# Optimization experiments

Measured on AMD Instinct MI355X. Metric: run time of the kernel, lower is better.

The kernel has to match this reference:

```python
import jax, jax.numpy as jnp
import numpy as np

N = 200000
D_NODE = 256
D_EDGE = 128
D_OUT = 256
J = 17


def setup_inputs() -> dict:
    key = jax.random.key(0)
    ks = jax.random.split(key, 16)
    s = 0.02
    return {
        "nodes_1": jax.random.normal(ks[0], (N, D_NODE), jnp.float32),
        "nodes_2": jax.random.normal(ks[1], (N, D_NODE), jnp.float32),
        "edges": jax.random.normal(ks[2], (N, D_EDGE), jnp.float32),
        "node_types_1": jax.random.randint(ks[3], (N,), 0, J),
        "node_types_2": jax.random.randint(ks[4], (N,), 0, J),
        # per-joint linear stacks (torch Linear weight [out,in] stored transposed as [in,out])
        "W1": jax.random.normal(ks[5], (J, D_NODE, D_OUT), jnp.float32) * s,
        "b1": jax.random.normal(ks[6], (J, D_OUT), jnp.float32) * s,
        "W2": jax.random.normal(ks[7], (J, D_NODE, D_OUT), jnp.float32) * s,
        "b2": jax.random.normal(ks[8], (J, D_OUT), jnp.float32) * s,
        "We": jax.random.normal(ks[9], (D_EDGE, D_OUT), jnp.float32) * s,
        "be": jax.random.normal(ks[10], (D_OUT,), jnp.float32) * s,
        "Wout": jax.random.normal(ks[11], (3 * D_OUT, D_OUT), jnp.float32) * s,
        "bout": jax.random.normal(ks[12], (D_OUT,), jnp.float32) * s,
    }


def _per_type_linear(nodes, types, W, b):
    # Equivalent to: for each joint i, tmp[types==i] = nodes[types==i] @ W[i] + b[i]
    out = jnp.zeros((nodes.shape[0], W.shape[2]), nodes.dtype)
    for i in range(W.shape[0]):  # small fixed loop over joint types
        yi = nodes @ W[i] + b[i]
        out = jnp.where((types == i)[:, None], yi, out)
    return out


def reference(nodes_1, nodes_2, edges, node_types_1, node_types_2,
              W1, b1, W2, b2, We, be, Wout, bout):
    tmp_1 = _per_type_linear(nodes_1, node_types_1, W1, b1)
    tmp_2 = _per_type_linear(nodes_2, node_types_2, W2, b2)
    e = edges @ We + be
    cat = jnp.concatenate([tmp_1, tmp_2, e], axis=1)  # [N, 3*D_OUT]
    h = jax.nn.relu(cat) @ Wout + bout
    return jax.nn.relu(h)
```

## Files before the change

kernel.cpp:

```cpp
#include <hip/hip_runtime.h>


#define J_TYPES 17
#define PAIRS   (J_TYPES * J_TYPES)
#define DN      256
#define DE      128
#define DO      256
#define TILE    64
#define LDA     264
#define LDE     136

typedef short bf16x8 __attribute__((ext_vector_type(8)));
typedef float f32x4  __attribute__((ext_vector_type(4)));

#define BAR() asm volatile("s_waitcnt lgkmcnt(0)\n\ts_barrier" ::: "memory")

__device__ __forceinline__ unsigned short f2bf(float x) {
  unsigned u = __float_as_uint(x);
  return (unsigned short)((u + 0x7fffu + ((u >> 16) & 1u)) >> 16);
}

__device__ __forceinline__ unsigned cvtpk(float lo, float hi) {
  unsigned r;
  asm("v_cvt_pk_bf16_f32 %0, %1, %2" : "=v"(r) : "v"(lo), "v"(hi));
  return r;
}

__global__ void prep_w_k(const float* __restrict__ W1, const float* __restrict__ W2,
                         const float* __restrict__ We, const float* __restrict__ Wout,
                         unsigned short* __restrict__ W1t, unsigned short* __restrict__ W2t,
                         unsigned short* __restrict__ Wet, unsigned short* __restrict__ Ut) {
  const int SZW = J_TYPES * 65536;
  const int total = SZW * 2 + DE * DO + 3 * 65536;
  for (int o = blockIdx.x * blockDim.x + threadIdx.x; o < total;
       o += gridDim.x * blockDim.x) {
    int idx = o;
    if (idx < SZW) {
      int j = idx >> 16, r = idx & 65535;
      int i = r & 7, lane = (r >> 3) & 63, t = r >> 9;
      int k32 = t & 7, colt = t >> 3;
      int col = colt * 16 + (lane & 15);
      int k = k32 * 32 + ((lane >> 4) << 3) + i;
      W1t[idx] = f2bf(W1[((size_t)j * 256 + k) * 256 + col]);
    } else if ((idx -= SZW) < SZW) {
      int j = idx >> 16, r = idx & 65535;
      int i = r & 7, lane = (r >> 3) & 63, t = r >> 9;
      int k32 = t & 7, colt = t >> 3;
      int col = colt * 16 + (lane & 15);
      int k = k32 * 32 + ((lane >> 4) << 3) + i;
      W2t[idx] = f2bf(W2[((size_t)j * 256 + k) * 256 + col]);
    } else if ((idx -= SZW) < DE * DO) {
      int r = idx;
      int i = r & 7, lane = (r >> 3) & 63, t = r >> 9;
      int k32 = t & 3, colt = t >> 2;
      int col = colt * 16 + (lane & 15);
      int k = k32 * 32 + ((lane >> 4) << 3) + i;
      Wet[idx] = f2bf(We[(size_t)k * 256 + col]);
    } else {
      idx -= DE * DO;
      int p = idx >> 16, r = idx & 65535;
      int i = r & 7, lane = (r >> 3) & 63, t = r >> 9;
      int k32 = t & 7, colt = t >> 3;
      int col = colt * 16 + (lane & 15);
      int k = k32 * 32 + ((lane >> 4) << 3) + i;
      Ut[idx] = f2bf(Wout[((size_t)p * 256 + k) * 256 + col]);
    }
  }
}

__global__ void hist_k(const int* __restrict__ ty1, const int* __restrict__ ty2,
                       int* __restrict__ cnt, int N) {
  __shared__ int h[PAIRS];
  for (int i = threadIdx.x; i < PAIRS; i += blockDim.x) h[i] = 0;
  __syncthreads();
  for (int i = blockIdx.x * blockDim.x + threadIdx.x; i < N;
       i += gridDim.x * blockDim.x)
    atomicAdd(&h[ty1[i] * J_TYPES + ty2[i]], 1);
  __syncthreads();
  for (int i = threadIdx.x; i < PAIRS; i += blockDim.x) {
    int v = h[i];
    if (v) atomicAdd(&cnt[i], v);
  }
}

__global__ void scan_tiles_k(const int* __restrict__ cnt, int* __restrict__ seg,
                             int* __restrict__ tpair, int* __restrict__ tstart,
                             int* __restrict__ tnr, int* __restrict__ ntl) {
  __shared__ int s1[512], s2[512];
  int t = threadIdx.x;
  int c  = (t < PAIRS) ? cnt[t] : 0;
  int nt = (c + TILE - 1) / TILE;
  s1[t] = c; s2[t] = nt;
  __syncthreads();
  for (int o = 1; o < 512; o <<= 1) {
    int v1 = (t >= o) ? s1[t - o] : 0;
    int v2 = (t >= o) ? s2[t - o] : 0;
    __syncthreads();
    s1[t] += v1; s2[t] += v2;
    __syncthreads();
  }
  if (t < PAIRS) {
    int segstart = s1[t] - c;
    int tbase    = s2[t] - nt;
    seg[t] = segstart;
    for (int i = 0; i < nt; ++i) {
      tpair[tbase + i]  = t;
      tstart[tbase + i] = segstart + i * TILE;
      int rem = c - i * TILE;
      tnr[tbase + i] = rem < TILE ? rem : TILE;
    }
  }
  if (t == 511) ntl[0] = s2[511];
}

__global__ void scatter_k(const int* __restrict__ ty1, const int* __restrict__ ty2,
                          const int* __restrict__ seg, int* __restrict__ c2,
                          int* __restrict__ ridx, int N) {
  __shared__ int lh[PAIRS], lb[PAIRS];
  int chunk = (N + gridDim.x - 1) / gridDim.x;
  int lo = blockIdx.x * chunk;
  int hi = lo + chunk; if (hi > N) hi = N;
  for (int i = threadIdx.x; i < PAIRS; i += blockDim.x) lh[i] = 0;
  __syncthreads();
  for (int i = lo + threadIdx.x; i < hi; i += blockDim.x)
    atomicAdd(&lh[ty1[i] * J_TYPES + ty2[i]], 1);
  __syncthreads();
  for (int i = threadIdx.x; i < PAIRS; i += blockDim.x) {
    int v = lh[i];
    lb[i] = v ? atomicAdd(&c2[i], v) : 0;
    lh[i] = 0;
  }
  __syncthreads();
  for (int i = lo + threadIdx.x; i < hi; i += blockDim.x) {
    int p = ty1[i] * J_TYPES + ty2[i];
    int pos = seg[p] + lb[p] + atomicAdd(&lh[p], 1);
    ridx[pos] = i;
  }
}


__device__ __forceinline__ void stage256(const float* __restrict__ src,
                                         const int* __restrict__ ridxp, int nrows,
                                         unsigned short* lds, int wave, int lane) {
  float4 f[8];
#pragma unroll
  for (int j = 0; j < 8; ++j) {
    int r = wave + 8 * j;
    int rc = r < nrows ? r : nrows - 1;
    int sr = ridxp[rc];
    f[j] = reinterpret_cast<const float4*>(src + (size_t)sr * DN)[lane];
  }
#pragma unroll
  for (int j = 0; j < 8; ++j) {
    int r = wave + 8 * j;
    unsigned lo = cvtpk(f[j].x, f[j].y), hi = cvtpk(f[j].z, f[j].w);
    *reinterpret_cast<uint2*>(lds + r * LDA + lane * 4) = make_uint2(lo, hi);
  }
}

__device__ __forceinline__ void stage128(const float* __restrict__ src,
                                         const int* __restrict__ ridxp, int nrows,
                                         unsigned short* lds, int wave, int lane) {
  float2 f[8];
#pragma unroll
  for (int j = 0; j < 8; ++j) {
    int r = wave + 8 * j;
    int rc = r < nrows ? r : nrows - 1;
    int sr = ridxp[rc];
    f[j] = reinterpret_cast<const float2*>(src + (size_t)sr * DE)[lane];
  }
#pragma unroll
  for (int j = 0; j < 8; ++j) {
    int r = wave + 8 * j;
    *reinterpret_cast<unsigned*>(lds + r * LDE + lane * 2) = cvtpk(f[j].x, f[j].y);
  }
}

template <int NK, int LD>
__device__ __forceinline__ void gemm32(const unsigned short* lds,
                                       const unsigned short* __restrict__ Wbase,
                                       f32x4 acc[4][2], int r0, int kg, int lane,
                                       int wave) {
  const unsigned short* w = Wbase + ((size_t)(wave * 2) * NK) * 512 + lane * 8;
  const int kw = wave & (NK - 1);
  bf16x8 bf[2][2], af[2][4];
#pragma unroll
  for (int cs = 0; cs < 2; ++cs)
    bf[0][cs] = *reinterpret_cast<const bf16x8*>(w + ((size_t)cs * NK + kw) * 512);
#pragma unroll
  for (int rs = 0; rs < 4; ++rs)
    af[0][rs] = *reinterpret_cast<const bf16x8*>(lds + (rs * 16 + r0) * LD + kw * 32 + kg);
#pragma unroll
  for (int i = 0; i < NK; ++i) {
    const int cur = i & 1, nxt = cur ^ 1;
    if (i + 1 < NK) {
      const int kk1 = (i + 1 + wave) & (NK - 1);
#pragma unroll
      for (int cs = 0; cs < 2; ++cs)
        bf[nxt][cs] =
            *reinterpret_cast<const bf16x8*>(w + ((size_t)cs * NK + kk1) * 512);
#pragma unroll
      for (int rs = 0; rs < 4; ++rs)
        af[nxt][rs] =
            *reinterpret_cast<const bf16x8*>(lds + (rs * 16 + r0) * LD + kk1 * 32 + kg);
    }
    __builtin_amdgcn_s_setprio(1);
#pragma unroll
    for (int rs = 0; rs < 4; ++rs)
#pragma unroll
      for (int cs = 0; cs < 2; ++cs)
        acc[rs][cs] = __builtin_amdgcn_mfma_f32_16x16x32_bf16(af[cur][rs], bf[cur][cs],
                                                              acc[rs][cs], 0, 0, 0);
    __builtin_amdgcn_s_setprio(0);
  }
}

__device__ __forceinline__ void epi32(f32x4 accT[4][2], const float* __restrict__ bias,
                                      unsigned short* ldsT, int r0, int rb, int wave) {
#pragma unroll
  for (int cs = 0; cs < 2; ++cs) {
    int col = wave * 32 + cs * 16 + r0;
    float b = bias[col];
#pragma unroll
    for (int rs = 0; rs < 4; ++rs) {
      float x0 = fmaxf(accT[rs][cs][0] + b, 0.f);
      float x1 = fmaxf(accT[rs][cs][1] + b, 0.f);
      float x2 = fmaxf(accT[rs][cs][2] + b, 0.f);
      float x3 = fmaxf(accT[rs][cs][3] + b, 0.f);
      unsigned w01 = cvtpk(x0, x1), w23 = cvtpk(x2, x3);
      int row = rs * 16 + rb;
      ldsT[(row + 0) * LDA + col] = (unsigned short)w01;
      ldsT[(row + 1) * LDA + col] = (unsigned short)(w01 >> 16);
      ldsT[(row + 2) * LDA + col] = (unsigned short)w23;
      ldsT[(row + 3) * LDA + col] = (unsigned short)(w23 >> 16);
    }
  }
}

#define ZERO42(A)                                                        \
  _Pragma("unroll") for (int a_ = 0; a_ < 4; ++a_) _Pragma("unroll")     \
      for (int b_ = 0; b_ < 2; ++b_) A[a_][b_] = (f32x4){0.f, 0.f, 0.f, 0.f};

__global__ __launch_bounds__(512, 4) void fused_k(
    const float* __restrict__ n1, const float* __restrict__ n2,
    const float* __restrict__ eg, const unsigned short* __restrict__ W1t,
    const unsigned short* __restrict__ W2t, const unsigned short* __restrict__ Wet,
    const unsigned short* __restrict__ Ut, const float* __restrict__ b1,
    const float* __restrict__ b2, const float* __restrict__ be,
    const float* __restrict__ bout, const int* __restrict__ ridx,
    const int* __restrict__ tpair, const int* __restrict__ tstart,
    const int* __restrict__ tnr, const int* __restrict__ ntl,
    float* __restrict__ out) {
  int nwg = gridDim.x, orig = blockIdx.x;
  int q = nwg >> 3, rr = nwg & 7, xc = orig & 7, sidx = orig >> 3;
  int tile = (xc < rr ? xc * (q + 1) : rr * (q + 1) + (xc - rr) * q) + sidx;
  if (tile >= ntl[0]) return;

  const int pr = tpair[tile];
  const int t1 = pr / J_TYPES, t2 = pr % J_TYPES;
  const int ts = tstart[tile];
  const int nrows = tnr[tile];
  const int* __restrict__ ridxp = ridx + ts;

  __shared__ unsigned short ldsA[TILE * LDA];
  __shared__ unsigned short ldsT[TILE * LDA];
  __shared__ int srow[TILE];

  const int lane = threadIdx.x & 63;
  const int wave = __builtin_amdgcn_readfirstlane(threadIdx.x >> 6);
  const int r0 = lane & 15;
  const int kg = (lane >> 4) * 8;
  const int rb = (lane >> 4) * 4;

  if (threadIdx.x < TILE)
    srow[threadIdx.x] = (threadIdx.x < nrows) ? ridxp[threadIdx.x] : -1;

  f32x4 accT[4][2], accO[4][2];

  stage256(n1, ridxp, nrows, ldsA, wave, lane);
  BAR();

  ZERO42(accT);
  gemm32<8, LDA>(ldsA, W1t + (size_t)t1 * 65536, accT, r0, kg, lane, wave);
  BAR();

  epi32(accT, b1 + t1 * 256, ldsT, r0, rb, wave);
  stage256(n2, ridxp, nrows, ldsA, wave, lane);
  BAR();

  ZERO42(accO);
  gemm32<8, LDA>(ldsT, Ut, accO, r0, kg, lane, wave);
  ZERO42(accT);
  gemm32<8, LDA>(ldsA, W2t + (size_t)t2 * 65536, accT, r0, kg, lane, wave);
  BAR();

  epi32(accT, b2 + t2 * 256, ldsT, r0, rb, wave);
  stage128(eg, ridxp, nrows, ldsA, wave, lane);
  BAR();

  gemm32<8, LDA>(ldsT, Ut + 65536, accO, r0, kg, lane, wave);
  ZERO42(accT);
  gemm32<4, LDE>(ldsA, Wet, accT, r0, kg, lane, wave);
  BAR();

  epi32(accT, be, ldsT, r0, rb, wave);
  BAR();

  gemm32<8, LDA>(ldsT, Ut + 2 * 65536, accO, r0, kg, lane, wave);

#pragma unroll
  for (int cs = 0; cs < 2; ++cs) {
    int col = wave * 32 + cs * 16 + r0;
    float bo = bout[col];
#pragma unroll
    for (int rs = 0; rs < 4; ++rs)
#pragma unroll
      for (int i = 0; i < 4; ++i) {
        int row = rs * 16 + rb + i;
        if (row < nrows) {
          float v = fmaxf(accO[rs][cs][i] + bo, 0.f);
          out[(size_t)srow[row] * 256 + col] = v;
        }
      }
  }
}

extern "C" void kernel_launch(void* const* d_in, const int* in_sizes, int n_in,
                              void* d_out, int out_size, void* d_ws, size_t ws_size,
                              hipStream_t stream) {
  const float* n1   = (const float*)d_in[0];
  const float* n2   = (const float*)d_in[1];
  const float* eg   = (const float*)d_in[2];
  const int*   ty1  = (const int*)d_in[3];
  const int*   ty2  = (const int*)d_in[4];
  const float* W1   = (const float*)d_in[5];
  const float* b1   = (const float*)d_in[6];
  const float* W2   = (const float*)d_in[7];
  const float* b2   = (const float*)d_in[8];
  const float* We   = (const float*)d_in[9];
  const float* be   = (const float*)d_in[10];
  const float* Wout = (const float*)d_in[11];
  const float* bout = (const float*)d_in[12];
  float* out = (float*)d_out;

  const int N = in_sizes[0] / DN;
  const int maxt = (N + TILE - 1) / TILE + PAIRS;

  char* ws = (char*)d_ws;
  size_t off = 0;
  auto take = [&](size_t bytes) -> char* {
    char* p = ws + off;
    off += (bytes + 255) & ~(size_t)255;
    return p;
  };
  int* cnt = (int*)take(PAIRS * 4);
  int* c2  = (int*)take(PAIRS * 4);
  int* ntl = (int*)take(4);
  int* seg = (int*)take((PAIRS + 1) * 4);
  int* tp  = (int*)take((size_t)maxt * 4);
  int* tst = (int*)take((size_t)maxt * 4);
  int* tnr = (int*)take((size_t)maxt * 4);
  int* ridx = (int*)take((size_t)N * 4);
  unsigned short* W1t = (unsigned short*)take((size_t)J_TYPES * 65536 * 2);
  unsigned short* W2t = (unsigned short*)take((size_t)J_TYPES * 65536 * 2);
  unsigned short* Wet = (unsigned short*)take((size_t)DE * DO * 2);
  unsigned short* Ut  = (unsigned short*)take((size_t)3 * 65536 * 2);
  (void)ws_size; (void)n_in; (void)out_size;

  hipMemsetAsync(cnt, 0, (size_t)((char*)seg - (char*)cnt), stream);
  prep_w_k<<<1024, 256, 0, stream>>>(W1, W2, We, Wout, W1t, W2t, Wet, Ut);
  hist_k<<<400, 256, 0, stream>>>(ty1, ty2, cnt, N);
  scan_tiles_k<<<1, 512, 0, stream>>>(cnt, seg, tp, tst, tnr, ntl);
  scatter_k<<<256, 256, 0, stream>>>(ty1, ty2, seg, c2, ridx, N);
  fused_k<<<maxt, 512, 0, stream>>>(n1, n2, eg, W1t, W2t, Wet, Ut, b1, b2, be, bout,
                                    ridx, tp, tst, tnr, ntl, out);
}
```

Baseline: 330.1 us.

## Prefetch next gathered input into registers during GEMM with double-buffered LDS

The gathered global loads for nodes_2 and edges are now issued before the preceding GEMM and written to a second LDS buffer afterwards, so load latency overlaps with MFMA work. The staging input buffer is doubled, and launch bounds drop from 4 to 2 blocks per SM so the extra prefetch registers fit. In exchange, occupancy falls and LDS use grows, which may cost the latency hiding that came from more resident blocks. An extra barrier is added between the epilogue and the next GEMM.

```diff
diff --git a/kernel.cpp b/kernel.cpp
--- a/kernel.cpp
+++ b/kernel.cpp
@@ -139,10 +139,9 @@
 }
 
 
-__device__ __forceinline__ void stage256(const float* __restrict__ src,
-                                         const int* __restrict__ ridxp, int nrows,
-                                         unsigned short* lds, int wave, int lane) {
-  float4 f[8];
+__device__ __forceinline__ void stage_issue256(const float* __restrict__ src,
+                                               const int* __restrict__ ridxp, int nrows,
+                                               int wave, int lane, float4 f[8]) {
 #pragma unroll
   for (int j = 0; j < 8; ++j) {
     int r = wave + 8 * j;
@@ -150,6 +149,10 @@
     int sr = ridxp[rc];
     f[j] = reinterpret_cast<const float4*>(src + (size_t)sr * DN)[lane];
   }
+}
+
+__device__ __forceinline__ void stage_write256(const float4 f[8],
+                                               unsigned short* lds, int wave, int lane) {
 #pragma unroll
   for (int j = 0; j < 8; ++j) {
     int r = wave + 8 * j;
@@ -158,10 +161,9 @@
   }
 }
 
-__device__ __forceinline__ void stage128(const float* __restrict__ src,
-                                         const int* __restrict__ ridxp, int nrows,
-                                         unsigned short* lds, int wave, int lane) {
-  float2 f[8];
+__device__ __forceinline__ void stage_issue128(const float* __restrict__ src,
+                                               const int* __restrict__ ridxp, int nrows,
+                                               int wave, int lane, float2 f[8]) {
 #pragma unroll
   for (int j = 0; j < 8; ++j) {
     int r = wave + 8 * j;
@@ -169,6 +171,10 @@
     int sr = ridxp[rc];
     f[j] = reinterpret_cast<const float2*>(src + (size_t)sr * DE)[lane];
   }
+}
+
+__device__ __forceinline__ void stage_write128(const float2 f[8],
+                                               unsigned short* lds, int wave, int lane) {
 #pragma unroll
   for (int j = 0; j < 8; ++j) {
     int r = wave + 8 * j;
@@ -241,7 +247,7 @@
   _Pragma("unroll") for (int a_ = 0; a_ < 4; ++a_) _Pragma("unroll")     \
       for (int b_ = 0; b_ < 2; ++b_) A[a_][b_] = (f32x4){0.f, 0.f, 0.f, 0.f};
 
-__global__ __launch_bounds__(512, 4) void fused_k(
+__global__ __launch_bounds__(512, 2) void fused_k(
     const float* __restrict__ n1, const float* __restrict__ n2,
     const float* __restrict__ eg, const unsigned short* __restrict__ W1t,
     const unsigned short* __restrict__ W2t, const unsigned short* __restrict__ Wet,
@@ -262,7 +268,7 @@
   const int nrows = tnr[tile];
   const int* __restrict__ ridxp = ridx + ts;
 
-  __shared__ unsigned short ldsA[TILE * LDA];
+  __shared__ unsigned short ldsA[2][TILE * LDA];
   __shared__ unsigned short ldsT[TILE * LDA];
   __shared__ int srow[TILE];
 
@@ -276,31 +282,36 @@
     srow[threadIdx.x] = (threadIdx.x < nrows) ? ridxp[threadIdx.x] : -1;
 
   f32x4 accT[4][2], accO[4][2];
-
-  stage256(n1, ridxp, nrows, ldsA, wave, lane);
-  BAR();
-
+  float4 f4[8];
+  float2 f2[8];
+
+  stage_issue256(n1, ridxp, nrows, wave, lane, f4);
+  stage_write256(f4, ldsA[0], wave, lane);
+  BAR();
+
+  stage_issue256(n2, ridxp, nrows, wave, lane, f4);
   ZERO42(accT);
-  gemm32<8, LDA>(ldsA, W1t + (size_t)t1 * 65536, accT, r0, kg, lane, wave);
+  gemm32<8, LDA>(ldsA[0], W1t + (size_t)t1 * 65536, accT, r0, kg, lane, wave);
+  stage_write256(f4, ldsA[1], wave, lane);
   BAR();
 
   epi32(accT, b1 + t1 * 256, ldsT, r0, rb, wave);
-  stage256(n2, ridxp, nrows, ldsA, wave, lane);
-  BAR();
-
+  BAR();
+
+  stage_issue128(eg, ridxp, nrows, wave, lane, f2);
   ZERO42(accO);
   gemm32<8, LDA>(ldsT, Ut, accO, r0, kg, lane, wave);
   ZERO42(accT);
-  gemm32<8, LDA>(ldsA, W2t + (size_t)t2 * 65536, accT, r0, kg, lane, wave);
+  gemm32<8, LDA>(ldsA[1], W2t + (size_t)t2 * 65536, accT, r0, kg, lane, wave);
+  stage_write128(f2, ldsA[0], wave, lane);
   BAR();
 
   epi32(accT, b2 + t2 * 256, ldsT, r0, rb, wave);
-  stage128(eg, ridxp, nrows, ldsA, wave, lane);
   BAR();
 
   gemm32<8, LDA>(ldsT, Ut + 65536, accO, r0, kg, lane, wave);
   ZERO42(accT);
-  gemm32<4, LDE>(ldsA, Wet, accT, r0, kg, lane, wave);
+  gemm32<4, LDE>(ldsA[0], Wet, accT, r0, kg, lane, wave);
   BAR();
 
   epi32(accT, be, ldsT, r0, rb, wave);
```

Measured after the change: 394.8 us. 1.2x slower.
